# Performance work log

Hardware: AMD Instinct MI355X
Metric: run time of the kernel (lower is better)

The kernel has to match this reference:

```python
import jax, jax.numpy as jnp
import numpy as np

H = 64
EPS = 1e-5


def _lstm_layer(x, w_ih, w_hh, b_ih, b_hh):
    """Single LSTM layer, batch_first input x: [B, T, I]. PyTorch gate order i,f,g,o."""
    B, T, _ = x.shape
    # precompute input contributions for all timesteps: [B, T, 4H]
    xw = jnp.einsum('bti,gi->btg', x, w_ih) + (b_ih + b_hh)
    xw = jnp.swapaxes(xw, 0, 1)  # [T, B, 4H] for scan over time

    def step(carry, xw_t):
        h, c = carry
        gates = xw_t + h @ w_hh.T  # [B, 4H]
        i, f, g, o = jnp.split(gates, 4, axis=-1)
        i = jax.nn.sigmoid(i)
        f = jax.nn.sigmoid(f)
        g = jnp.tanh(g)
        o = jax.nn.sigmoid(o)
        c = f * c + i * g
        h = o * jnp.tanh(c)
        return (h, c), h

    h0 = jnp.zeros((B, H), x.dtype)
    (_, _), hs = jax.lax.scan(step, (h0, h0), xw)
    return jnp.swapaxes(hs, 0, 1)  # [B, T, H]


def setup_inputs() -> dict:
    key = jax.random.key(0)
    ks = jax.random.split(key, 16)
    B, T, F = 4096, 256, 32
    s = 1.0 / np.sqrt(H)  # PyTorch LSTM init scale
    inp = {
        'x': jax.random.normal(ks[0], (B, T, F), jnp.float32),
        'w_ih0': jax.random.uniform(ks[1], (4 * H, F), jnp.float32, -s, s),
        'w_hh0': jax.random.uniform(ks[2], (4 * H, H), jnp.float32, -s, s),
        'b_ih0': jax.random.uniform(ks[3], (4 * H,), jnp.float32, -s, s),
        'b_hh0': jax.random.uniform(ks[4], (4 * H,), jnp.float32, -s, s),
        'w_ih1': jax.random.uniform(ks[5], (4 * H, H), jnp.float32, -s, s),
        'w_hh1': jax.random.uniform(ks[6], (4 * H, H), jnp.float32, -s, s),
        'b_ih1': jax.random.uniform(ks[7], (4 * H,), jnp.float32, -s, s),
        'b_hh1': jax.random.uniform(ks[8], (4 * H,), jnp.float32, -s, s),
        'ln_g': jnp.ones((H,), jnp.float32),
        'ln_b': jnp.zeros((H,), jnp.float32),
        'w1': jax.random.uniform(ks[9], (64, H), jnp.float32, -s, s),
        'b1': jax.random.uniform(ks[10], (64,), jnp.float32, -s, s),
        'w2': jax.random.uniform(ks[11], (1, 64), jnp.float32, -0.125, 0.125),
        'b2': jax.random.uniform(ks[12], (1,), jnp.float32, -0.125, 0.125),
    }
    return inp


def reference(x, w_ih0, w_hh0, b_ih0, b_hh0, w_ih1, w_hh1, b_ih1, b_hh1,
              ln_g, ln_b, w1, b1, w2, b2):
    out0 = _lstm_layer(x, w_ih0, w_hh0, b_ih0, b_hh0)      # [B, T, H]
    out1 = _lstm_layer(out0, w_ih1, w_hh1, b_ih1, b_hh1)   # [B, T, H]
    last = out1[:, -1, :]                                   # [B, H]
    # LayerNorm
    mu = jnp.mean(last, axis=-1, keepdims=True)
    var = jnp.mean(jnp.square(last - mu), axis=-1, keepdims=True)
    ln = (last - mu) * jax.lax.rsqrt(var + EPS) * ln_g + ln_b
    # MLP head
    h = jax.nn.relu(ln @ w1.T + b1)
    y = h @ w2.T + b2                                       # [B, 1]
    return y[:, 0]
```

## Files before the change

### kernel.cpp

```cpp
#include <hip/hip_runtime.h>

#define TSEQ 256
#define FIN  32
#define HID  64

#define LOG2E    1.4426950408889634f
#define TWOLOG2E 2.8853900817779268f

typedef _Float16 f16x8 __attribute__((ext_vector_type(8)));
typedef __fp16   h16x2 __attribute__((ext_vector_type(2)));
typedef float    f32x4 __attribute__((ext_vector_type(4)));

#if __has_builtin(__builtin_amdgcn_exp2f)
__device__ __forceinline__ float fast_exp2(float x) { return __builtin_amdgcn_exp2f(x); }
#else
extern "C" __device__ float __ocml_native_exp2_f32(float);
__device__ __forceinline__ float fast_exp2(float x) { return __ocml_native_exp2_f32(x); }
#endif

#define BAR_LDS() do { asm volatile("s_waitcnt lgkmcnt(0)" ::: "memory"); \
                       __builtin_amdgcn_s_barrier(); } while (0)

__device__ __forceinline__ float wsum(float v) {
    #pragma unroll
    for (int off = 32; off > 0; off >>= 1) v += __shfl_xor(v, off, 64);
    return v;
}

__device__ __forceinline__ float lstm_cell(const f32x4 g, float& c) {
    float ei = fast_exp2(g[0]);
    float ef = fast_exp2(g[1]);
    float yg = fast_exp2(g[2]);
    float eo = fast_exp2(g[3]);
    float t1 = 1.0f + ei;
    float t2 = 1.0f + ef;
    float p  = t1 * (yg + 1.0f);
    float r  = __builtin_amdgcn_rcpf(p * t2);
    float ig = (yg - 1.0f) * t2 * r;
    float sf = p * r;
    c = fmaf(sf, c, ig);
    float cc = __builtin_amdgcn_fmed3f(c, -15.0f, 15.0f);
    float yc = fast_exp2(TWOLOG2E * cc);
    return (yc - 1.0f) * __builtin_amdgcn_rcpf((1.0f + eo) * (yc + 1.0f));
}

__global__ __launch_bounds__(512, 2)
void lstm_fused(const float* __restrict__ x,
                const float* __restrict__ w_ih0, const float* __restrict__ w_hh0,
                const float* __restrict__ b_ih0, const float* __restrict__ b_hh0,
                const float* __restrict__ w_ih1, const float* __restrict__ w_hh1,
                const float* __restrict__ b_ih1, const float* __restrict__ b_hh1,
                const float* __restrict__ ln_g, const float* __restrict__ ln_b,
                const float* __restrict__ w1, const float* __restrict__ b1,
                const float* __restrict__ w2, const float* __restrict__ b2,
                float* __restrict__ out)
{
    __shared__ __align__(16) _Float16 H0[2][16][72];
    __shared__ __align__(16) _Float16 H1[2][16][72];
    __shared__ __align__(16) float HF[16][68];
    __shared__ __align__(16) float LNB[16][64];

    const int tid  = threadIdx.x;
    const int wave = tid >> 6;
    const int lane = tid & 63;
    const int q    = lane >> 4;
    const int lm   = lane & 15;
    const int q8   = q * 8;
    const int b0   = blockIdx.x * 16;

    const bool isA = wave < 4;
    const int  wt  = wave & 3;
    const int rbase = (lm & 3) * 64 + (lm >> 2);
    const int dq0   = wt * 16 + q;
    const float wsc = ((lm & 3) == 2) ? TWOLOG2E : -LOG2E;

    f16x8 wf[16];
    f32x4 biasv[4];
    if (isA) {
        #pragma unroll
        for (int t = 0; t < 4; ++t) {
            const int row = rbase + wt * 16 + t * 4;
            const float* p0 = w_ih0 + row * FIN + q8;
            const float* p1 = w_hh0 + row * HID + q8;
            const float* p2 = p1 + 32;
            #pragma unroll
            for (int j = 0; j < 8; ++j) {
                wf[t * 3 + 0][j] = (_Float16)(wsc * p0[j]);
                wf[t * 3 + 1][j] = (_Float16)(wsc * p1[j]);
                wf[t * 3 + 2][j] = (_Float16)(wsc * p2[j]);
            }
            const int d = dq0 + t * 4;
            #pragma unroll
            for (int r = 0; r < 4; ++r) {
                const float s = (r == 2) ? TWOLOG2E : -LOG2E;
                biasv[t][r] = s * (b_ih0[r * 64 + d] + b_hh0[r * 64 + d]);
            }
        }
    } else {
        #pragma unroll
        for (int t = 0; t < 4; ++t) {
            const int row = rbase + wt * 16 + t * 4;
            const float* p0 = w_ih1 + row * HID + q8;
            const float* p1 = p0 + 32;
            const float* p2 = w_hh1 + row * HID + q8;
            const float* p3 = p2 + 32;
            #pragma unroll
            for (int j = 0; j < 8; ++j) {
                wf[t * 4 + 0][j] = (_Float16)(wsc * p0[j]);
                wf[t * 4 + 1][j] = (_Float16)(wsc * p1[j]);
                wf[t * 4 + 2][j] = (_Float16)(wsc * p2[j]);
                wf[t * 4 + 3][j] = (_Float16)(wsc * p3[j]);
            }
            const int d = dq0 + t * 4;
            #pragma unroll
            for (int r = 0; r < 4; ++r) {
                const float s = (r == 2) ? TWOLOG2E : -LOG2E;
                biasv[t][r] = s * (b_ih1[r * 64 + d] + b_hh1[r * 64 + d]);
            }
        }
    }

    const float* xp = x + (size_t)(b0 + lm) * TSEQ * FIN + q8;
    f32x4 xfa, xfb;
    if (isA) {
        xfa = *reinterpret_cast<const f32x4*>(xp);
        xfb = *reinterpret_cast<const f32x4*>(xp + 4);
    }

    for (int i = tid; i < 2 * 16 * 72; i += 512) {
        ((_Float16*)H0)[i] = (_Float16)0.0f;
        ((_Float16*)H1)[i] = (_Float16)0.0f;
    }
    float cs0 = 0.0f, cs1 = 0.0f, cs2 = 0.0f, cs3 = 0.0f;
    float lastB0 = 0.0f, lastB1 = 0.0f, lastB2 = 0.0f, lastB3 = 0.0f;
    __syncthreads();

#define MFMA __builtin_amdgcn_mfma_f32_16x16x32_f16
#define INTERVAL(P, DO_A, DO_B, DO_XL, XI)                                          \
    {                                                                               \
        if (isA) {                                                                  \
            f16x8 xcur;                                                             \
            {                                                                       \
                h16x2 c0_ = __builtin_amdgcn_cvt_pkrtz(xfa[0], xfa[1]);             \
                h16x2 c1_ = __builtin_amdgcn_cvt_pkrtz(xfa[2], xfa[3]);             \
                h16x2 c2_ = __builtin_amdgcn_cvt_pkrtz(xfb[0], xfb[1]);             \
                h16x2 c3_ = __builtin_amdgcn_cvt_pkrtz(xfb[2], xfb[3]);             \
                xcur[0] = (_Float16)c0_[0]; xcur[1] = (_Float16)c0_[1];             \
                xcur[2] = (_Float16)c1_[0]; xcur[3] = (_Float16)c1_[1];             \
                xcur[4] = (_Float16)c2_[0]; xcur[5] = (_Float16)c2_[1];             \
                xcur[6] = (_Float16)c3_[0]; xcur[7] = (_Float16)c3_[1];             \
            }                                                                       \
            if (DO_XL) {                                                            \
                xfa = *reinterpret_cast<const f32x4*>(xp + (size_t)(XI) * FIN);     \
                xfb = *reinterpret_cast<const f32x4*>(xp + (size_t)(XI) * FIN + 4); \
            }                                                                       \
            if (DO_A) {                                                             \
                f32x4 a0 = biasv[0], a1 = biasv[1], a2 = biasv[2], a3 = biasv[3];   \
                   \
                a0 = MFMA(wf[0], xcur, a0, 0, 0, 0);                                \
                a1 = MFMA(wf[3], xcur, a1, 0, 0, 0);                                \
                a2 = MFMA(wf[6], xcur, a2, 0, 0, 0);                                \
                a3 = MFMA(wf[9], xcur, a3, 0, 0, 0);                                \
                f16x8 rh0a = *reinterpret_cast<const f16x8*>(&H0[(P) ^ 1][lm][q8]);      \
                f16x8 rh0b = *reinterpret_cast<const f16x8*>(&H0[(P) ^ 1][lm][32 + q8]); \
                a0 = MFMA(wf[1],  rh0a, a0, 0, 0, 0);                               \
                a1 = MFMA(wf[4],  rh0a, a1, 0, 0, 0);                               \
                a2 = MFMA(wf[7],  rh0a, a2, 0, 0, 0);                               \
                a3 = MFMA(wf[10], rh0a, a3, 0, 0, 0);                               \
                a0 = MFMA(wf[2],  rh0b, a0, 0, 0, 0);                               \
                a1 = MFMA(wf[5],  rh0b, a1, 0, 0, 0);                               \
                a2 = MFMA(wf[8],  rh0b, a2, 0, 0, 0);                               \
                a3 = MFMA(wf[11], rh0b, a3, 0, 0, 0);                               \
                float hv0 = lstm_cell(a0, cs0);                                     \
                float hv1 = lstm_cell(a1, cs1);                                     \
                float hv2 = lstm_cell(a2, cs2);                                     \
                float hv3 = lstm_cell(a3, cs3);                                     \
                H0[P][lm][dq0]      = (_Float16)hv0;                                \
                H0[P][lm][dq0 + 4]  = (_Float16)hv1;                                \
                H0[P][lm][dq0 + 8]  = (_Float16)hv2;                                \
                H0[P][lm][dq0 + 12] = (_Float16)hv3;                                \
            }                                                                       \
        } else if (DO_B) {                                                          \
            f16x8 rh0a = *reinterpret_cast<const f16x8*>(&H0[(P) ^ 1][lm][q8]);      \
            f16x8 rh0b = *reinterpret_cast<const f16x8*>(&H0[(P) ^ 1][lm][32 + q8]); \
            f32x4 a0 = biasv[0], a1 = biasv[1], a2 = biasv[2], a3 = biasv[3];       \
            a0 = MFMA(wf[0],  rh0a, a0, 0, 0, 0);                                   \
            a1 = MFMA(wf[4],  rh0a, a1, 0, 0, 0);                                   \
            a2 = MFMA(wf[8],  rh0a, a2, 0, 0, 0);                                   \
            a3 = MFMA(wf[12], rh0a, a3, 0, 0, 0);                                   \
            a0 = MFMA(wf[1],  rh0b, a0, 0, 0, 0);                                   \
            a1 = MFMA(wf[5],  rh0b, a1, 0, 0, 0);                                   \
            a2 = MFMA(wf[9],  rh0b, a2, 0, 0, 0);                                   \
            a3 = MFMA(wf[13], rh0b, a3, 0, 0, 0);                                   \
            f16x8 rh1a = *reinterpret_cast<const f16x8*>(&H1[P][lm][q8]);            \
            f16x8 rh1b = *reinterpret_cast<const f16x8*>(&H1[P][lm][32 + q8]);       \
            a0 = MFMA(wf[2],  rh1a, a0, 0, 0, 0);                                   \
            a1 = MFMA(wf[6],  rh1a, a1, 0, 0, 0);                                   \
            a2 = MFMA(wf[10], rh1a, a2, 0, 0, 0);                                   \
            a3 = MFMA(wf[14], rh1a, a3, 0, 0, 0);                                   \
            a0 = MFMA(wf[3],  rh1b, a0, 0, 0, 0);                                   \
            a1 = MFMA(wf[7],  rh1b, a1, 0, 0, 0);                                   \
            a2 = MFMA(wf[11], rh1b, a2, 0, 0, 0);                                   \
            a3 = MFMA(wf[15], rh1b, a3, 0, 0, 0);                                   \
            float hv0 = lstm_cell(a0, cs0);                                         \
            float hv1 = lstm_cell(a1, cs1);                                         \
            float hv2 = lstm_cell(a2, cs2);                                         \
            float hv3 = lstm_cell(a3, cs3);                                         \
            H1[(P) ^ 1][lm][dq0]      = (_Float16)hv0;                              \
            H1[(P) ^ 1][lm][dq0 + 4]  = (_Float16)hv1;                              \
            H1[(P) ^ 1][lm][dq0 + 8]  = (_Float16)hv2;                              \
            H1[(P) ^ 1][lm][dq0 + 12] = (_Float16)hv3;                              \
            lastB0 = hv0; lastB1 = hv1; lastB2 = hv2; lastB3 = hv3;                 \
        }                                                                           \
        BAR_LDS();                                                                  \
    }

    INTERVAL(0, true, false, true, 1)

    #pragma unroll 1
    for (int ii = 0; ii < 127; ++ii) {
        const int i1 = 2 * ii + 1;
        INTERVAL(1, true, true, true, i1 + 1)
        INTERVAL(0, true, true, true, i1 + 2)
    }

    INTERVAL(1, true, true, false, 0)
    INTERVAL(0, false, true, false, 0)

#undef INTERVAL
#undef MFMA

    if (!isA) {
        HF[lm][dq0]      = lastB0;
        HF[lm][dq0 + 4]  = lastB1;
        HF[lm][dq0 + 8]  = lastB2;
        HF[lm][dq0 + 12] = lastB3;
    }
    __syncthreads();

    const float lngv = ln_g[lane], lnbv = ln_b[lane];
    const float b1v = b1[lane], w2v = w2[lane];
    const float* w1row = w1 + lane * 64;
    #pragma unroll
    for (int rr = wave; rr < 16; rr += 8) {
        float v  = HF[rr][lane];
        float mu = wsum(v) * (1.0f / 64.0f);
        float dv = v - mu;
        float var = wsum(dv * dv) * (1.0f / 64.0f);
        float ln = dv * rsqrtf(var + 1e-5f) * lngv + lnbv;
        LNB[rr][lane] = ln;
        float s = b1v;
        #pragma unroll
        for (int dd = 0; dd < 64; ++dd)
            s = fmaf(LNB[rr][dd], w1row[dd], s);
        s = fmaxf(s, 0.0f);
        float y = wsum(s * w2v);
        if (lane == 0) out[b0 + rr] = y + b2[0];
    }
}

extern "C" void kernel_launch(void* const* d_in, const int* in_sizes, int n_in,
                              void* d_out, int out_size, void* d_ws, size_t ws_size,
                              hipStream_t stream) {
    const float* x     = (const float*)d_in[0];
    const float* w_ih0 = (const float*)d_in[1];
    const float* w_hh0 = (const float*)d_in[2];
    const float* b_ih0 = (const float*)d_in[3];
    const float* b_hh0 = (const float*)d_in[4];
    const float* w_ih1 = (const float*)d_in[5];
    const float* w_hh1 = (const float*)d_in[6];
    const float* b_ih1 = (const float*)d_in[7];
    const float* b_hh1 = (const float*)d_in[8];
    const float* ln_g  = (const float*)d_in[9];
    const float* ln_b  = (const float*)d_in[10];
    const float* w1    = (const float*)d_in[11];
    const float* b1    = (const float*)d_in[12];
    const float* w2    = (const float*)d_in[13];
    const float* b2    = (const float*)d_in[14];
    lstm_fused<<<dim3(256), dim3(512), 0, stream>>>(
        x, w_ih0, w_hh0, b_ih0, b_hh0,
        w_ih1, w_hh1, b_ih1, b_hh1,
        ln_g, ln_b, w1, b1, w2, b2, (float*)d_out);
}
```

Baseline: 361.9 us.

## Split each LSTM step into MFMA and cell phases across two barriers

Each interval now has two barrier-separated halves. Layer-0 waves issue their MFMAs in the first half and run the cell nonlinearity in the second. Layer-1 waves do the reverse, running the cell on the previous step's accumulators first and then issuing MFMAs, so the MFMA work of one wave group overlaps the transcendental math of the other. The cost is a second barrier per step, an extra pipeline stage in the prologue and epilogue with shifted indexing, and more live registers for the carried layer-1 accumulators.

Result: slower. 399.5 us (+10.4%).

```diff
diff --git a/kernel.cpp b/kernel.cpp
--- a/kernel.cpp
+++ b/kernel.cpp
@@ -132,100 +132,108 @@
         ((_Float16*)H1)[i] = (_Float16)0.0f;
     }
     float cs0 = 0.0f, cs1 = 0.0f, cs2 = 0.0f, cs3 = 0.0f;
+    f32x4 hb0 = {0,0,0,0}, hb1 = {0,0,0,0}, hb2 = {0,0,0,0}, hb3 = {0,0,0,0};
     float lastB0 = 0.0f, lastB1 = 0.0f, lastB2 = 0.0f, lastB3 = 0.0f;
     __syncthreads();
 
 #define MFMA __builtin_amdgcn_mfma_f32_16x16x32_f16
-#define INTERVAL(P, DO_A, DO_B, DO_XL, XI)                                          \
+#define INTERVAL(P, DO_A, DO_BC, DO_BM, XI)                                         \
     {                                                                               \
+        f32x4 g0 = biasv[0], g1 = biasv[1], g2 = biasv[2], g3 = biasv[3];           \
+                   \
         if (isA) {                                                                  \
-            f16x8 xcur;                                                             \
-            {                                                                       \
-                h16x2 c0_ = __builtin_amdgcn_cvt_pkrtz(xfa[0], xfa[1]);             \
-                h16x2 c1_ = __builtin_amdgcn_cvt_pkrtz(xfa[2], xfa[3]);             \
-                h16x2 c2_ = __builtin_amdgcn_cvt_pkrtz(xfb[0], xfb[1]);             \
-                h16x2 c3_ = __builtin_amdgcn_cvt_pkrtz(xfb[2], xfb[3]);             \
-                xcur[0] = (_Float16)c0_[0]; xcur[1] = (_Float16)c0_[1];             \
-                xcur[2] = (_Float16)c1_[0]; xcur[3] = (_Float16)c1_[1];             \
-                xcur[4] = (_Float16)c2_[0]; xcur[5] = (_Float16)c2_[1];             \
-                xcur[6] = (_Float16)c3_[0]; xcur[7] = (_Float16)c3_[1];             \
-            }                                                                       \
-            if (DO_XL) {                                                            \
+            if (DO_A) {                                                             \
+                f16x8 xcur;                                                         \
+                {                                                                   \
+                    h16x2 c0_ = __builtin_amdgcn_cvt_pkrtz(xfa[0], xfa[1]);         \
+                    h16x2 c1_ = __builtin_amdgcn_cvt_pkrtz(xfa[2], xfa[3]);         \
+                    h16x2 c2_ = __builtin_amdgcn_cvt_pkrtz(xfb[0], xfb[1]);         \
+                    h16x2 c3_ = __builtin_amdgcn_cvt_pkrtz(xfb[2], xfb[3]);         \
+                    xcur[0] = (_Float16)c0_[0]; xcur[1] = (_Float16)c0_[1];         \
+                    xcur[2] = (_Float16)c1_[0]; xcur[3] = (_Float16)c1_[1];         \
+                    xcur[4] = (_Float16)c2_[0]; xcur[5] = (_Float16)c2_[1];         \
+                    xcur[6] = (_Float16)c3_[0]; xcur[7] = (_Float16)c3_[1];         \
+                }                                                                   \
                 xfa = *reinterpret_cast<const f32x4*>(xp + (size_t)(XI) * FIN);     \
                 xfb = *reinterpret_cast<const f32x4*>(xp + (size_t)(XI) * FIN + 4); \
-            }                                                                       \
-            if (DO_A) {                                                             \
-                f32x4 a0 = biasv[0], a1 = biasv[1], a2 = biasv[2], a3 = biasv[3];   \
-                   \
-                a0 = MFMA(wf[0], xcur, a0, 0, 0, 0);                                \
-                a1 = MFMA(wf[3], xcur, a1, 0, 0, 0);                                \
-                a2 = MFMA(wf[6], xcur, a2, 0, 0, 0);                                \
-                a3 = MFMA(wf[9], xcur, a3, 0, 0, 0);                                \
+                g0 = MFMA(wf[0], xcur, g0, 0, 0, 0);                                \
+                g1 = MFMA(wf[3], xcur, g1, 0, 0, 0);                                \
+                g2 = MFMA(wf[6], xcur, g2, 0, 0, 0);                                \
+                g3 = MFMA(wf[9], xcur, g3, 0, 0, 0);                                \
                 f16x8 rh0a = *reinterpret_cast<const f16x8*>(&H0[(P) ^ 1][lm][q8]);      \
                 f16x8 rh0b = *reinterpret_cast<const f16x8*>(&H0[(P) ^ 1][lm][32 + q8]); \
-                a0 = MFMA(wf[1],  rh0a, a0, 0, 0, 0);                               \
-                a1 = MFMA(wf[4],  rh0a, a1, 0, 0, 0);                               \
-                a2 = MFMA(wf[7],  rh0a, a2, 0, 0, 0);                               \
-                a3 = MFMA(wf[10], rh0a, a3, 0, 0, 0);                               \
-                a0 = MFMA(wf[2],  rh0b, a0, 0, 0, 0);                               \
-                a1 = MFMA(wf[5],  rh0b, a1, 0, 0, 0);                               \
-                a2 = MFMA(wf[8],  rh0b, a2, 0, 0, 0);                               \
-                a3 = MFMA(wf[11], rh0b, a3, 0, 0, 0);                               \
-                float hv0 = lstm_cell(a0, cs0);                                     \
-                float hv1 = lstm_cell(a1, cs1);                                     \
-                float hv2 = lstm_cell(a2, cs2);                                     \
-                float hv3 = lstm_cell(a3, cs3);                                     \
+                g0 = MFMA(wf[1],  rh0a, g0, 0, 0, 0);                               \
+                g1 = MFMA(wf[4],  rh0a, g1, 0, 0, 0);                               \
+                g2 = MFMA(wf[7],  rh0a, g2, 0, 0, 0);                               \
+                g3 = MFMA(wf[10], rh0a, g3, 0, 0, 0);                               \
+                g0 = MFMA(wf[2],  rh0b, g0, 0, 0, 0);                               \
+                g1 = MFMA(wf[5],  rh0b, g1, 0, 0, 0);                               \
+                g2 = MFMA(wf[8],  rh0b, g2, 0, 0, 0);                               \
+                g3 = MFMA(wf[11], rh0b, g3, 0, 0, 0);                               \
+            }                                                                       \
+        } else if (DO_BC) {                                                         \
+            float hv0 = lstm_cell(hb0, cs0);                                        \
+            float hv1 = lstm_cell(hb1, cs1);                                        \
+            float hv2 = lstm_cell(hb2, cs2);                                        \
+            float hv3 = lstm_cell(hb3, cs3);                                        \
+            H1[P][lm][dq0]      = (_Float16)hv0;                                    \
+            H1[P][lm][dq0 + 4]  = (_Float16)hv1;                                    \
+            H1[P][lm][dq0 + 8]  = (_Float16)hv2;                                    \
+            H1[P][lm][dq0 + 12] = (_Float16)hv3;                                    \
+            lastB0 = hv0; lastB1 = hv1; lastB2 = hv2; lastB3 = hv3;                 \
+        }                                                                           \
+        BAR_LDS();                                                                  \
+                   \
+        if (isA) {                                                                  \
+            if (DO_A) {                                                             \
+                float hv0 = lstm_cell(g0, cs0);                                     \
+                float hv1 = lstm_cell(g1, cs1);                                     \
+                float hv2 = lstm_cell(g2, cs2);                                     \
+                float hv3 = lstm_cell(g3, cs3);                                     \
                 H0[P][lm][dq0]      = (_Float16)hv0;                                \
                 H0[P][lm][dq0 + 4]  = (_Float16)hv1;                                \
                 H0[P][lm][dq0 + 8]  = (_Float16)hv2;                                \
                 H0[P][lm][dq0 + 12] = (_Float16)hv3;                                \
             }                                                                       \
-        } else if (DO_B) {                                                          \
+        } else if (DO_BM) {                                                         \
             f16x8 rh0a = *reinterpret_cast<const f16x8*>(&H0[(P) ^ 1][lm][q8]);      \
             f16x8 rh0b = *reinterpret_cast<const f16x8*>(&H0[(P) ^ 1][lm][32 + q8]); \
-            f32x4 a0 = biasv[0], a1 = biasv[1], a2 = biasv[2], a3 = biasv[3];       \
-            a0 = MFMA(wf[0],  rh0a, a0, 0, 0, 0);                                   \
-            a1 = MFMA(wf[4],  rh0a, a1, 0, 0, 0);                                   \
-            a2 = MFMA(wf[8],  rh0a, a2, 0, 0, 0);                                   \
-            a3 = MFMA(wf[12], rh0a, a3, 0, 0, 0);                                   \
-            a0 = MFMA(wf[1],  rh0b, a0, 0, 0, 0);                                   \
-            a1 = MFMA(wf[5],  rh0b, a1, 0, 0, 0);                                   \
-            a2 = MFMA(wf[9],  rh0b, a2, 0, 0, 0);                                   \
-            a3 = MFMA(wf[13], rh0b, a3, 0, 0, 0);                                   \
             f16x8 rh1a = *reinterpret_cast<const f16x8*>(&H1[P][lm][q8]);            \
             f16x8 rh1b = *reinterpret_cast<const f16x8*>(&H1[P][lm][32 + q8]);       \
-            a0 = MFMA(wf[2],  rh1a, a0, 0, 0, 0);                                   \
-            a1 = MFMA(wf[6],  rh1a, a1, 0, 0, 0);                                   \
-            a2 = MFMA(wf[10], rh1a, a2, 0, 0, 0);                                   \
-            a3 = MFMA(wf[14], rh1a, a3, 0, 0, 0);                                   \
-            a0 = MFMA(wf[3],  rh1b, a0, 0, 0, 0);                                   \
-            a1 = MFMA(wf[7],  rh1b, a1, 0, 0, 0);                                   \
-            a2 = MFMA(wf[11], rh1b, a2, 0, 0, 0);                                   \
-            a3 = MFMA(wf[15], rh1b, a3, 0, 0, 0);                                   \
-            float hv0 = lstm_cell(a0, cs0);                                         \
-            float hv1 = lstm_cell(a1, cs1);                                         \
-            float hv2 = lstm_cell(a2, cs2);                                         \
-            float hv3 = lstm_cell(a3, cs3);                                         \
-            H1[(P) ^ 1][lm][dq0]      = (_Float16)hv0;                              \
-            H1[(P) ^ 1][lm][dq0 + 4]  = (_Float16)hv1;                              \
-            H1[(P) ^ 1][lm][dq0 + 8]  = (_Float16)hv2;                              \
-            H1[(P) ^ 1][lm][dq0 + 12] = (_Float16)hv3;                              \
-            lastB0 = hv0; lastB1 = hv1; lastB2 = hv2; lastB3 = hv3;                 \
+            hb0 = biasv[0]; hb1 = biasv[1]; hb2 = biasv[2]; hb3 = biasv[3];         \
+            hb0 = MFMA(wf[0],  rh0a, hb0, 0, 0, 0);                                 \
+            hb1 = MFMA(wf[4],  rh0a, hb1, 0, 0, 0);                                 \
+            hb2 = MFMA(wf[8],  rh0a, hb2, 0, 0, 0);                                 \
+            hb3 = MFMA(wf[12], rh0a, hb3, 0, 0, 0);                                 \
+            hb0 = MFMA(wf[1],  rh0b, hb0, 0, 0, 0);                                 \
+            hb1 = MFMA(wf[5],  rh0b, hb1, 0, 0, 0);                                 \
+            hb2 = MFMA(wf[9],  rh0b, hb2, 0, 0, 0);                                 \
+            hb3 = MFMA(wf[13], rh0b, hb3, 0, 0, 0);                                 \
+            hb0 = MFMA(wf[2],  rh1a, hb0, 0, 0, 0);                                 \
+            hb1 = MFMA(wf[6],  rh1a, hb1, 0, 0, 0);                                 \
+            hb2 = MFMA(wf[10], rh1a, hb2, 0, 0, 0);                                 \
+            hb3 = MFMA(wf[14], rh1a, hb3, 0, 0, 0);                                 \
+            hb0 = MFMA(wf[3],  rh1b, hb0, 0, 0, 0);                                 \
+            hb1 = MFMA(wf[7],  rh1b, hb1, 0, 0, 0);                                 \
+            hb2 = MFMA(wf[11], rh1b, hb2, 0, 0, 0);                                 \
+            hb3 = MFMA(wf[15], rh1b, hb3, 0, 0, 0);                                 \
         }                                                                           \
         BAR_LDS();                                                                  \
     }
 
-    INTERVAL(0, true, false, true, 1)
+    INTERVAL(0, true, false, false, 1)
+    INTERVAL(1, true, false, true, 2)
 
     #pragma unroll 1
     for (int ii = 0; ii < 127; ++ii) {
-        const int i1 = 2 * ii + 1;
-        INTERVAL(1, true, true, true, i1 + 1)
-        INTERVAL(0, true, true, true, i1 + 2)
-    }
-
-    INTERVAL(1, true, true, false, 0)
-    INTERVAL(0, false, true, false, 0)
+        const int i0 = 2 * ii + 2;
+        const int xiB = (i0 + 2 > 255) ? 255 : i0 + 2;
+        INTERVAL(0, true, true, true, i0 + 1)
+        INTERVAL(1, true, true, true, xiB)
+    }
+
+    INTERVAL(0, false, true, true, 0)
+    INTERVAL(1, false, true, false, 0)
 
 #undef INTERVAL
 #undef MFMA
```
